# Optimization experiments

Hardware: AMD Instinct MI355X
Metric: run time of the kernel (lower is better)

## Reference

```python
import jax, jax.numpy as jnp
import numpy as np

B, S, H = 1, 4096, 2048
NH, NKV, HD = 16, 4, 128  # query heads, kv heads, head_dim
THETA = 1000000.0
NEG = -1e9


def setup_inputs() -> dict:
    key = jax.random.key(0)
    ks = jax.random.split(key, 5)
    hidden_states = jax.random.normal(ks[0], (B, S, H), jnp.float32) * 0.02
    Wq = jax.random.normal(ks[1], (H, NH * HD), jnp.float32) * 0.02
    Wk = jax.random.normal(ks[2], (H, NKV * HD), jnp.float32) * 0.02
    Wv = jax.random.normal(ks[3], (H, NKV * HD), jnp.float32) * 0.02
    Wo = jax.random.normal(ks[4], (H, H), jnp.float32) * 0.02
    # additive causal mask [B,1,S,S]
    causal = jnp.tril(jnp.ones((S, S), bool))
    attention_mask = jnp.where(causal, 0.0, NEG).astype(jnp.float32)[None, None]
    position_ids = jnp.arange(S, dtype=jnp.int32)[None]
    return dict(hidden_states=hidden_states, Wq=Wq, Wk=Wk, Wv=Wv, Wo=Wo,
                attention_mask=attention_mask, position_ids=position_ids)


def _rotate_half(x):
    return jnp.concatenate([-x[..., HD // 2:], x[..., :HD // 2]], axis=-1)


def reference(hidden_states, Wq, Wk, Wv, Wo, attention_mask, position_ids):
    # projections -> [B, heads, S, HD]
    q = (hidden_states @ Wq).reshape(B, S, NH, HD).transpose(0, 2, 1, 3)
    k = (hidden_states @ Wk).reshape(B, S, NKV, HD).transpose(0, 2, 1, 3)
    v = (hidden_states @ Wv).reshape(B, S, NKV, HD).transpose(0, 2, 1, 3)

    # RoPE (HF style: freqs duplicated across halves, rotate_half)
    inv_freq = 1.0 / (THETA ** (jnp.arange(0, HD, 2, dtype=jnp.float32) / HD))
    freqs = position_ids.astype(jnp.float32)[..., None] * inv_freq  # [B,S,HD/2]
    emb = jnp.concatenate([freqs, freqs], axis=-1)                  # [B,S,HD]
    cos = jnp.cos(emb)[:, None].astype(q.dtype)                     # [B,1,S,HD]
    sin = jnp.sin(emb)[:, None].astype(q.dtype)
    q = q * cos + _rotate_half(q) * sin
    k = k * cos + _rotate_half(k) * sin

    # GQA: repeat each kv head consecutively (matches torch repeat_kv)
    rep = NH // NKV
    k = jnp.repeat(k, rep, axis=1)
    v = jnp.repeat(v, rep, axis=1)

    scale = 1.0 / jnp.sqrt(jnp.float32(HD))
    scores = jnp.einsum('bhqd,bhkd->bhqk', q, k) * scale + attention_mask
    attn = jax.nn.softmax(scores.astype(jnp.float32), axis=-1).astype(q.dtype)
    out = jnp.einsum('bhqk,bhkd->bhqd', attn, v)  # [B,NH,S,HD]
    out = out.transpose(0, 2, 1, 3).reshape(B, S, H)
    return out @ Wo
```

## Files before the change

### kernel.cpp

```cpp
#include <hip/hip_runtime.h>
#include <stdint.h>

typedef uint16_t u16;
typedef __bf16  bf16x8 __attribute__((ext_vector_type(8)));
typedef float   f32x4  __attribute__((ext_vector_type(4)));
typedef float   f32x16 __attribute__((ext_vector_type(16)));
typedef uint16_t u16x8 __attribute__((ext_vector_type(8), may_alias));
typedef uint32_t u32x4 __attribute__((ext_vector_type(4)));

typedef const __attribute__((address_space(1))) void* gas_p;
typedef __attribute__((address_space(3))) void* las_p;

#define SCALE2 0.1275430214486847f

__device__ __forceinline__ void load_lds16(const void* g, void* l) {
    __builtin_amdgcn_global_load_lds((gas_p)g, (las_p)l, 16, 0, 0);
}

__device__ __forceinline__ u16 f2bf(float f) {
    uint32_t u = __builtin_bit_cast(uint32_t, f);
    u += 0x7FFFu + ((u >> 16) & 1u);
    return (u16)(u >> 16);
}
__device__ __forceinline__ float bf2f(u16 h) {
    uint32_t u = ((uint32_t)h) << 16;
    return __builtin_bit_cast(float, u);
}
__device__ __forceinline__ bf16x8 ld_frag(const u16* p) {
    u16x8 t = *(const u16x8*)p;
    return __builtin_bit_cast(bf16x8, t);
}
__device__ __forceinline__ uint32_t cvt_pk_bf16(float lo, float hi) {
    uint32_t r;
    asm("v_cvt_pk_bf16_f32 %0, %1, %2" : "=v"(r) : "v"(lo), "v"(hi));
    return r;
}
__device__ __forceinline__ void plane32_swap(uint32_t& a, uint32_t& b) {
    asm("v_permlane32_swap_b32 %0, %1" : "+v"(a), "+v"(b));
}

__global__ __launch_bounds__(256) void convert_hidden(const float* __restrict__ in,
                                                      u16* __restrict__ out, int n8) {
    int i = blockIdx.x * 256 + threadIdx.x;
    if (i >= n8) return;
    const float* p = in + (size_t)i * 8;
    u16x8 o;
#pragma unroll
    for (int j = 0; j < 8; j++) o[j] = f2bf(p[j]);
    *(u16x8*)(out + (size_t)i * 8) = o;
}

__global__ __launch_bounds__(256) void transpose_cvt(const float* __restrict__ in,
                                                     u16* __restrict__ out,
                                                     int R, int C) {
    __shared__ u16 tile[64][65];
    const int tx = threadIdx.x;
    const int bc = blockIdx.x * 64;
    const int br = blockIdx.y * 64;
#pragma unroll
    for (int i = 0; i < 16; i++) {
        int idx = tx + i * 256;
        int r = idx >> 6, c = idx & 63;
        tile[r][c] = f2bf(in[(size_t)(br + r) * C + bc + c]);
    }
    __syncthreads();
#pragma unroll
    for (int i = 0; i < 16; i++) {
        int idx = tx + i * 256;
        int r = idx >> 6, c = idx & 63;
        out[(size_t)(bc + r) * R + br + c] = tile[c][r];
    }
}

__global__ __launch_bounds__(256) void transpose_b16(const u16* __restrict__ in,
                                                     u16* __restrict__ out,
                                                     int R, int C, int ldin, int off) {
    __shared__ u16 tile[64][65];
    const int tx = threadIdx.x;
    const int bc = blockIdx.x * 64;
    const int br = blockIdx.y * 64;
#pragma unroll
    for (int i = 0; i < 16; i++) {
        int idx = tx + i * 256;
        int r = idx >> 6, c = idx & 63;
        tile[r][c] = in[(size_t)(br + r) * ldin + off + bc + c];
    }
    __syncthreads();
#pragma unroll
    for (int i = 0; i < 16; i++) {
        int idx = tx + i * 256;
        int r = idx >> 6, c = idx & 63;
        out[(size_t)(bc + r) * R + br + c] = tile[c][r];
    }
}

#define TM 128
#define TN 128
#define TK 32

__global__ __launch_bounds__(256) void gemm_qkv(const u16* __restrict__ A,
                                                const u16* __restrict__ WqT,
                                                const u16* __restrict__ WkvT,
                                                u16* __restrict__ Qb,
                                                u16* __restrict__ KVb) {
    __shared__ u16 As[TM * TK];
    __shared__ u16 Bs[TN * TK];
    const int K = 2048;
    const int tid  = threadIdx.x;
    const int wave = tid >> 6;
    const int lane = tid & 63;
    const int l15  = lane & 15;
    const int quad = lane >> 4;
    const int m0 = blockIdx.y * TM;
    const int n0 = blockIdx.x * TN;
    const u16* Bt;
    u16* C;
    int ldC, cbase;
    if (n0 < 2048) { Bt = WqT + (size_t)n0 * K;          C = Qb;  ldC = 2048; cbase = n0; }
    else           { Bt = WkvT + (size_t)(n0 - 2048) * K; C = KVb; ldC = 1024; cbase = n0 - 2048; }
    const int wm = (wave >> 1) * 64;
    const int wn = (wave & 1) * 64;

    f32x4 acc[4][4] = {};

    const int srow = tid >> 2;
    const int scol = (tid & 3) * 8;
    const u16* Ap0 = A  + (size_t)(m0 + srow) * K + scol;
    const u16* Ap1 = A  + (size_t)(m0 + 64 + srow) * K + scol;
    const u16* Bp0 = Bt + (size_t)srow * K + scol;
    const u16* Bp1 = Bt + (size_t)(64 + srow) * K + scol;
    u16* AsD0 = As + wave * 512;
    u16* AsD1 = As + 2048 + wave * 512;
    u16* BsD0 = Bs + wave * 512;
    u16* BsD1 = Bs + 2048 + wave * 512;

    for (int k0 = 0; k0 < K; k0 += TK) {
        load_lds16(Ap0 + k0, AsD0);
        load_lds16(Ap1 + k0, AsD1);
        load_lds16(Bp0 + k0, BsD0);
        load_lds16(Bp1 + k0, BsD1);
        __syncthreads();
        bf16x8 af[4], bfr[4];
#pragma unroll
        for (int i = 0; i < 4; i++)
            af[i] = ld_frag(&As[(wm + i * 16 + l15) * TK + quad * 8]);
#pragma unroll
        for (int j = 0; j < 4; j++)
            bfr[j] = ld_frag(&Bs[(wn + j * 16 + l15) * TK + quad * 8]);
#pragma unroll
        for (int i = 0; i < 4; i++)
#pragma unroll
            for (int j = 0; j < 4; j++)
                acc[i][j] = __builtin_amdgcn_mfma_f32_16x16x32_bf16(af[i], bfr[j], acc[i][j], 0, 0, 0);
        __syncthreads();
    }
#pragma unroll
    for (int i = 0; i < 4; i++)
#pragma unroll
        for (int j = 0; j < 4; j++)
#pragma unroll
            for (int r = 0; r < 4; r++) {
                int row = m0 + wm + i * 16 + quad * 4 + r;
                int col = cbase + wn + j * 16 + l15;
                C[(size_t)row * ldC + col] = f2bf(acc[i][j][r]);
            }
}

template <bool F32OUT>
__global__ __launch_bounds__(256) void gemm_bt(const u16* __restrict__ A,
                                               const u16* __restrict__ Bt,
                                               void* __restrict__ Cp,
                                               int M, int N, int K) {
    __shared__ u16 As[TM * TK];
    __shared__ u16 Bs[TN * TK];
    const int tid  = threadIdx.x;
    const int wave = tid >> 6;
    const int lane = tid & 63;
    const int l15  = lane & 15;
    const int quad = lane >> 4;
    const int m0 = blockIdx.y * TM;
    const int n0 = blockIdx.x * TN;
    const int wm = (wave >> 1) * 64;
    const int wn = (wave & 1) * 64;

    f32x4 acc[4][4] = {};

    const int srow = tid >> 2;
    const int scol = (tid & 3) * 8;
    const u16* Ap0 = A  + (size_t)(m0 + srow) * K + scol;
    const u16* Ap1 = A  + (size_t)(m0 + 64 + srow) * K + scol;
    const u16* Bp0 = Bt + (size_t)(n0 + srow) * K + scol;
    const u16* Bp1 = Bt + (size_t)(n0 + 64 + srow) * K + scol;
    u16* AsD0 = As + wave * 512;
    u16* AsD1 = As + 2048 + wave * 512;
    u16* BsD0 = Bs + wave * 512;
    u16* BsD1 = Bs + 2048 + wave * 512;

    for (int k0 = 0; k0 < K; k0 += TK) {
        load_lds16(Ap0 + k0, AsD0);
        load_lds16(Ap1 + k0, AsD1);
        load_lds16(Bp0 + k0, BsD0);
        load_lds16(Bp1 + k0, BsD1);
        __syncthreads();
        bf16x8 af[4], bfr[4];
#pragma unroll
        for (int i = 0; i < 4; i++)
            af[i] = ld_frag(&As[(wm + i * 16 + l15) * TK + quad * 8]);
#pragma unroll
        for (int j = 0; j < 4; j++)
            bfr[j] = ld_frag(&Bs[(wn + j * 16 + l15) * TK + quad * 8]);
#pragma unroll
        for (int i = 0; i < 4; i++)
#pragma unroll
            for (int j = 0; j < 4; j++)
                acc[i][j] = __builtin_amdgcn_mfma_f32_16x16x32_bf16(af[i], bfr[j], acc[i][j], 0, 0, 0);
        __syncthreads();
    }
#pragma unroll
    for (int i = 0; i < 4; i++)
#pragma unroll
        for (int j = 0; j < 4; j++)
#pragma unroll
            for (int r = 0; r < 4; r++) {
                int row = m0 + wm + i * 16 + quad * 4 + r;
                int col = n0 + wn + j * 16 + l15;
                if (F32OUT)
                    ((float*)Cp)[(size_t)row * N + col] = acc[i][j][r];
                else
                    ((u16*)Cp)[(size_t)row * N + col] = f2bf(acc[i][j][r]);
            }
}

__global__ __launch_bounds__(256) void rope_kernel(u16* __restrict__ Q,
                                                   u16* __restrict__ KV) {
    int g = blockIdx.x * 256 + threadIdx.x;
    int d = g & 63;
    int row = g >> 6;
    int s = row / 20;
    int hh = row - s * 20;
    u16* buf = (hh < 16) ? (Q + (size_t)s * 2048 + hh * 128)
                         : (KV + (size_t)s * 1024 + (hh - 16) * 128);
    float p = (float)s;
    float angle = p * exp2f((float)d * (-19.931568569324174f / 64.0f));
    float sc = (hh < 16) ? SCALE2 : 1.0f;
    float c = cosf(angle) * sc, sn = sinf(angle) * sc;
    float x0 = bf2f(buf[d]), x1 = bf2f(buf[d + 64]);
    buf[d]      = f2bf(x0 * c - x1 * sn);
    buf[d + 64] = f2bf(x1 * c + x0 * sn);
}


#define QK1(CC, MSK)                                                           \
  do {                                                                         \
    const int krow_ = (CC) * 32 + l31;                                         \
    f32x16 sv_ = {};                                                           \
    _Pragma("unroll")                                                          \
    for (int dk = 0; dk < 8; dk++) {                                           \
      bf16x8 kf = ld_frag(&Kb[krow_ * 128 + (((dk * 2 + hi8) + krow_) & 15) * 8]); \
      sv_ = __builtin_amdgcn_mfma_f32_32x32x16_bf16(kf, qf[dk], sv_, 0, 0, 0); \
    }                                                                          \
    float p_[16]; float rs_ = 0.f;                                             \
    const int kvbs_ = kv0 + (CC) * 32 + 4 * hi8;                               \
    _Pragma("unroll")                                                          \
    for (int r = 0; r < 16; r++) {                                             \
      float pe = exp2f(sv_[r]);                                                \
      if (MSK) { int kvv = kvbs_ + (r & 3) + 8 * (r >> 2);                     \
                 pe = (kvv <= qrow) ? pe : 0.f; }                              \
      p_[r] = pe; rs_ += pe;                                                   \
    }                                                                          \
    lr += rs_;                                                                 \
    uint32_t w0 = cvt_pk_bf16(p_[0], p_[1]);                                   \
    uint32_t w1 = cvt_pk_bf16(p_[2], p_[3]);                                   \
    uint32_t w2 = cvt_pk_bf16(p_[4], p_[5]);                                   \
    uint32_t w3 = cvt_pk_bf16(p_[6], p_[7]);                                   \
    plane32_swap(w0, w2); plane32_swap(w1, w3);                                \
    uint32_t w4 = cvt_pk_bf16(p_[8], p_[9]);                                   \
    uint32_t w5 = cvt_pk_bf16(p_[10], p_[11]);                                 \
    uint32_t w6 = cvt_pk_bf16(p_[12], p_[13]);                                 \
    plane32_swap(w4, w6);                                                      \
    uint32_t w7 = cvt_pk_bf16(p_[14], p_[15]);                                 \
    plane32_swap(w5, w7);                                                      \
    u32x4 a0_ = {w0, w1, w2, w3}, a1_ = {w4, w5, w6, w7};                      \
    bf16x8 pa0_ = __builtin_bit_cast(bf16x8, a0_);                             \
    bf16x8 pa1_ = __builtin_bit_cast(bf16x8, a1_);                             \
    _Pragma("unroll")                                                          \
    for (int ks2 = 0; ks2 < 2; ks2++) {                                        \
      bf16x8 pa_ = ks2 ? pa1_ : pa0_;                                          \
      _Pragma("unroll")                                                        \
      for (int nt = 0; nt < 4; nt++) {                                         \
        const int d_ = nt * 32 + l31;                                          \
        bf16x8 vf = ld_frag(&Vb[d_ * 64 + ((((CC) * 4 + ks2 * 2 + hi8) + d_) & 7) * 8]); \
        acc[nt] = __builtin_amdgcn_mfma_f32_32x32x16_bf16(pa_, vf, acc[nt], 0, 0, 0); \
      }                                                                        \
    }                                                                          \
  } while (0)

__global__ __launch_bounds__(256, 2) void flash_attn7(const u16* __restrict__ Q,
                                                      const u16* __restrict__ KVb,
                                                      const u16* __restrict__ VT,
                                                      u16* __restrict__ O) {
    __shared__ u16 Ks[2][8192];
    __shared__ u16 Vs[2][8192];
    __shared__ float Llds[4][32];
    const int tid  = threadIdx.x;
    const int ww   = tid >> 6;
    const int lane = tid & 63;
    const int l31  = lane & 31;
    const int hi8  = lane >> 5;
    const int bid  = blockIdx.x;
    const int h    = bid >> 5;
    const int cls  = bid & 31;
    const int bx   = cls >> 1;
    const int z    = cls & 1;
    const int kvh  = h >> 2;
    const int qt0  = z ? (3968 - bx * 128) : (bx * 128);
    const int qg0  = qt0 + ww * 32;
    const int qrow = qg0 + l31;
    const int dW   = qg0 >> 6;
    const int nkv  = (qt0 >> 6) + 2;

    bf16x8 qf[8];
    {
        const u16* qp = Q + (size_t)qrow * 2048 + h * 128 + hi8 * 8;
#pragma unroll
        for (int dk = 0; dk < 8; dk++) qf[dk] = ld_frag(qp + dk * 16);
    }

    const u16* srcK[4];
    const u16* srcV[4];
#pragma unroll
    for (int r = 0; r < 4; r++) {
        int p = r * 256 + tid;
        int kv = p >> 4;
        srcK[r] = KVb + (size_t)kv * 1024 + kvh * 128 + ((((p & 15) - kv) & 15) * 8);
        int d = p >> 3;
        srcV[r] = VT + (size_t)(kvh * 128 + d) * 4096 + ((((p & 7) - (d & 7)) & 7) * 8);
    }

    f32x16 acc[4] = {};
    float lr = 0.f;

#pragma unroll
    for (int r = 0; r < 4; r++) {
        load_lds16(srcK[r], &Ks[0][r * 2048 + ww * 512]);
        load_lds16(srcV[r], &Vs[0][r * 2048 + ww * 512]);
    }
    asm volatile("s_waitcnt vmcnt(0)" ::: "memory");
    __syncthreads();

    for (int kvb = 0; kvb < nkv; kvb++) {
        const int cur = kvb & 1;
        if (kvb + 1 < nkv) {
            const int kvn = (kvb + 1) * 64;
#pragma unroll
            for (int r = 0; r < 4; r++) {
                load_lds16(srcK[r] + (size_t)kvn * 1024, &Ks[cur ^ 1][r * 2048 + ww * 512]);
                load_lds16(srcV[r] + kvn, &Vs[cur ^ 1][r * 2048 + ww * 512]);
            }
        }
        const u16* Kb = Ks[cur];
        const u16* Vb = Vs[cur];
        const int kv0 = kvb * 64;

        if (kvb < dW) {
            QK1(0, 0);
            QK1(1, 0);
        } else if (kvb == dW) {
            QK1(0, 1);
            QK1(1, 1);
        }

        asm volatile("s_waitcnt vmcnt(0)" ::: "memory");
        __syncthreads();
    }

    float lt = lr + __shfl_xor(lr, 32);
    if (lane < 32) Llds[ww][l31] = lt;
    __syncthreads();
#pragma unroll
    for (int r = 0; r < 16; r++) {
        int qr = (r & 3) + 8 * (r >> 2) + 4 * hi8;
        float linv = 1.0f / Llds[ww][qr];
        u16* op = O + (size_t)(qg0 + qr) * 2048 + h * 128 + l31;
#pragma unroll
        for (int nt = 0; nt < 4; nt++)
            op[nt * 32] = f2bf(acc[nt][r] * linv);
    }
}

extern "C" void kernel_launch(void* const* d_in, const int* in_sizes, int n_in,
                              void* d_out, int out_size, void* d_ws, size_t ws_size,
                              hipStream_t stream) {
    const float* hidden = (const float*)d_in[0];
    const float* Wq = (const float*)d_in[1];
    const float* Wk = (const float*)d_in[2];
    const float* Wv = (const float*)d_in[3];
    const float* Wo = (const float*)d_in[4];
    float* out = (float*)d_out;

    u16* ws   = (u16*)d_ws;
    u16* Hb   = ws;
    u16* Qb   = Hb   + 8388608;
    u16* KVb  = Qb   + 8388608;
    u16* WqT  = KVb  + 4194304;
    u16* WkvT = WqT  + 4194304;
    u16* VT   = WkvT + 2097152;

    convert_hidden<<<4096, 256, 0, stream>>>(hidden, Hb, 1048576);

    transpose_cvt<<<dim3(32, 32), 256, 0, stream>>>(Wq, WqT, 2048, 2048);
    transpose_cvt<<<dim3(8, 32), 256, 0, stream>>>(Wk, WkvT, 2048, 512);
    transpose_cvt<<<dim3(8, 32), 256, 0, stream>>>(Wv, WkvT + 1048576, 2048, 512);

    gemm_qkv<<<dim3(24, 32), 256, 0, stream>>>(Hb, WqT, WkvT, Qb, KVb);

    u16* WoT = WqT;
    transpose_cvt<<<dim3(32, 32), 256, 0, stream>>>(Wo, WoT, 2048, 2048);

    rope_kernel<<<dim3(20480), 256, 0, stream>>>(Qb, KVb);

    transpose_b16<<<dim3(8, 64), 256, 0, stream>>>(KVb, VT, 4096, 512, 1024, 512);

    u16* Ob = Hb;
    flash_attn7<<<dim3(512), 256, 0, stream>>>(Qb, KVb, VT, Ob);

    gemm_bt<true><<<dim3(16, 32), 256, 0, stream>>>(Ob, WoT, out, 4096, 2048, 2048);
}
```

Before: 429.5 us.

## Split causal attention KV range in two blocks and merge partial outputs

Adds a split-KV flash attention kernel where each 128-row query tile's causal KV range is halved across two blocks, giving 1024 blocks ordered longest-first. Each block writes an unnormalized bf16 partial output plus row sums, and a merge kernel adds the partials and divides by the combined sum. This targets load imbalance and low parallelism in causal attention. In exchange it adds an extra kernel launch, extra global traffic for partials, and bf16 rounding of unnormalized partials. It runs only when the workspace is large enough. Both halves skip the running-max rescale, so they must share a fixed softmax reference for the merge to be valid.

```diff
diff --git a/kernel.cpp b/kernel.cpp
--- a/kernel.cpp
+++ b/kernel.cpp
@@ -248,7 +248,6 @@
     buf[d]      = f2bf(x0 * c - x1 * sn);
     buf[d + 64] = f2bf(x1 * c + x0 * sn);
 }
-
 
 #define QK1(CC, MSK)                                                           \
   do {                                                                         \
@@ -295,6 +294,116 @@
     }                                                                          \
   } while (0)
 
+__global__ __launch_bounds__(256, 2) void flash_attn9(const u16* __restrict__ Q,
+                                                      const u16* __restrict__ KVb,
+                                                      const u16* __restrict__ VT,
+                                                      u16* __restrict__ Op0,
+                                                      u16* __restrict__ Op1,
+                                                      float* __restrict__ Lp) {
+    __shared__ u16 Ks[2][8192];
+    __shared__ u16 Vs[2][8192];
+    const int tid  = threadIdx.x;
+    const int ww   = tid >> 6;
+    const int lane = tid & 63;
+    const int l31  = lane & 31;
+    const int hi8  = lane >> 5;
+    const int bid  = blockIdx.x;
+    const int h    = (bid & 7) * 2 + ((bid >> 3) & 1);
+    const int rest = bid >> 4;
+    const int j    = 31 - (rest >> 1);
+    const int s    = rest & 1;
+    const int kvh  = h >> 2;
+    const int qg0  = j * 128 + ww * 32;
+    const int qrow = qg0 + l31;
+    const int dW   = qg0 >> 6;
+    const int kb0  = s * (j + 1);
+    const int kb1  = kb0 + (j + 1);
+
+    bf16x8 qf[8];
+    {
+        const u16* qp = Q + (size_t)qrow * 2048 + h * 128 + hi8 * 8;
+#pragma unroll
+        for (int dk = 0; dk < 8; dk++) qf[dk] = ld_frag(qp + dk * 16);
+    }
+
+    const u16* srcK[4];
+    const u16* srcV[4];
+#pragma unroll
+    for (int r = 0; r < 4; r++) {
+        int p = r * 256 + tid;
+        int kv = p >> 4;
+        srcK[r] = KVb + (size_t)kv * 1024 + kvh * 128 + ((((p & 15) - kv) & 15) * 8);
+        int d = p >> 3;
+        srcV[r] = VT + (size_t)(kvh * 128 + d) * 4096 + ((((p & 7) - (d & 7)) & 7) * 8);
+    }
+
+    f32x16 acc[4] = {};
+    float lr = 0.f;
+
+#pragma unroll
+    for (int r = 0; r < 4; r++) {
+        load_lds16(srcK[r] + (size_t)(kb0 * 64) * 1024, &Ks[0][r * 2048 + ww * 512]);
+        load_lds16(srcV[r] + kb0 * 64, &Vs[0][r * 2048 + ww * 512]);
+    }
+    asm volatile("s_waitcnt vmcnt(0)" ::: "memory");
+    __syncthreads();
+
+    for (int kvb = kb0; kvb < kb1; kvb++) {
+        const int cur = (kvb - kb0) & 1;
+        if (kvb + 1 < kb1) {
+            const int kvn = (kvb + 1) * 64;
+#pragma unroll
+            for (int r = 0; r < 4; r++) {
+                load_lds16(srcK[r] + (size_t)kvn * 1024, &Ks[cur ^ 1][r * 2048 + ww * 512]);
+                load_lds16(srcV[r] + kvn, &Vs[cur ^ 1][r * 2048 + ww * 512]);
+            }
+        }
+        const u16* Kb = Ks[cur];
+        const u16* Vb = Vs[cur];
+        const int kv0 = kvb * 64;
+
+        if (kvb < dW) {
+            QK1(0, 0);
+            QK1(1, 0);
+        } else if (kvb == dW) {
+            QK1(0, 1);
+            QK1(1, 1);
+        }
+
+        asm volatile("s_waitcnt vmcnt(0)" ::: "memory");
+        __syncthreads();
+    }
+
+    float lt = lr + __shfl_xor(lr, 32);
+    if (lane < 32) Lp[(s * 16 + h) * 4096 + qg0 + l31] = lt;
+    u16* Ops = s ? Op1 : Op0;
+#pragma unroll
+    for (int r = 0; r < 16; r++) {
+        int qr = (r & 3) + 8 * (r >> 2) + 4 * hi8;
+        u16* op = Ops + (size_t)(qg0 + qr) * 2048 + h * 128 + l31;
+#pragma unroll
+        for (int nt = 0; nt < 4; nt++)
+            op[nt * 32] = f2bf(acc[nt][r]);
+    }
+}
+
+__global__ __launch_bounds__(256) void merge_o(u16* __restrict__ o0,
+                                               const u16* __restrict__ o1,
+                                               const float* __restrict__ Lp) {
+    int i = blockIdx.x * 256 + threadIdx.x;
+    size_t base = (size_t)i * 8;
+    int row = (int)(base >> 11);
+    int h   = (int)((base >> 7) & 15);
+    float inv = 1.0f / (Lp[h * 4096 + row] + Lp[(16 + h) * 4096 + row]);
+    u16x8 a = *(const u16x8*)(o0 + base);
+    u16x8 b = *(const u16x8*)(o1 + base);
+    u16x8 o;
+#pragma unroll
+    for (int jj = 0; jj < 8; jj++)
+        o[jj] = f2bf((bf2f(a[jj]) + bf2f(b[jj])) * inv);
+    *(u16x8*)(o0 + base) = o;
+}
+
 __global__ __launch_bounds__(256, 2) void flash_attn7(const u16* __restrict__ Q,
                                                       const u16* __restrict__ KVb,
                                                       const u16* __restrict__ VT,
@@ -405,6 +514,8 @@
     u16* WqT  = KVb  + 4194304;
     u16* WkvT = WqT  + 4194304;
     u16* VT   = WkvT + 2097152;
+    u16* Op1  = VT   + 4194304;
+    const size_t WS_SPLIT = (size_t)(31457280 + 8388608) * 2;
 
     convert_hidden<<<4096, 256, 0, stream>>>(hidden, Hb, 1048576);
 
@@ -422,7 +533,13 @@
     transpose_b16<<<dim3(8, 64), 256, 0, stream>>>(KVb, VT, 4096, 512, 1024, 512);
 
     u16* Ob = Hb;
-    flash_attn7<<<dim3(512), 256, 0, stream>>>(Qb, KVb, VT, Ob);
+    if (ws_size >= WS_SPLIT) {
+        float* Lp = (float*)WkvT;
+        flash_attn9<<<dim3(1024), 256, 0, stream>>>(Qb, KVb, VT, Ob, Op1, Lp);
+        merge_o<<<dim3(4096), 256, 0, stream>>>(Ob, Op1, Lp);
+    } else {
+        flash_attn7<<<dim3(512), 256, 0, stream>>>(Qb, KVb, VT, Ob);
+    }
 
     gemm_bt<true><<<dim3(16, 32), 256, 0, stream>>>(Ob, WoT, out, 4096, 2048, 2048);
 }
```

After: 388.0 us. 9.7% less time.
